# Optimization experiments

Hardware: AMD Instinct MI355X
Metric: run time of the kernel (lower is better)

The kernel has to match this reference:

```python
import jax, jax.numpy as jnp
import numpy as np

BITWIDTH = 8
Q_FRAC = BITWIDTH - 4                       # fractional bits of output quantizer
Q_SCALE = 2.0 ** Q_FRAC                     # 16
QMAX = (2 ** (BITWIDTH - 1) - 1) / Q_SCALE  # 7.9375 (overflow clamp on accumulator)
QMIN = -8.0                                 # underflow clamp / accumulator init
LUT_IN_SCALE = 4096.0                       # diff quantized to Q12 index
LUT_IN_MAX = 32767.0                        # index clamp
LUT_OUT_SCALE = 65536.0                     # look_up (= table/2) lives on a 1/65536 grid


def _lut(diff):
    # Emulates the hex lookup table: table[i]/2 ~= log(1 + exp(-i/4096)),
    # quantized to the 1/65536 grid (table entries are Q15, then halved).
    d_int = jnp.minimum(jnp.floor(diff * LUT_IN_SCALE), LUT_IN_MAX)
    d_q = d_int / LUT_IN_SCALE
    return jnp.round(jnp.log1p(jnp.exp(-d_q)) * LUT_OUT_SCALE) / LUT_OUT_SCALE


def _quant_feature(x):
    # QuantizeFeature(bitwidth, bitwidth-4): round to 1/16 grid, clamp to int8 range.
    q = jnp.clip(jnp.round(x * Q_SCALE), -(2 ** (BITWIDTH - 1)), 2 ** (BITWIDTH - 1) - 1)
    return q / Q_SCALE


def _quantized_log_softmax(x):
    B, C, H, W = x.shape
    flat = x.reshape(B * C, H, W)  # sequential axis = flattened batch*channel (as in source)
    init = jnp.full((H, W), QMIN, dtype=x.dtype)

    def step(sum_exp, t):  # t: [H, W]
        diff = jnp.abs(sum_exp - t)
        lu = _lut(diff)
        # if sum_exp > t: sum_exp += lu else: sum_exp = t + lu  ==  max(sum_exp, t) + lu
        s = jnp.maximum(sum_exp, t) + lu
        s = jnp.clip(s, QMIN, QMAX)  # overflow/underflow clamps
        return s, None

    sum_exp, _ = jax.lax.scan(step, init, flat)
    # final scalar per spatial location is broadcast to every (b, c)
    return _quant_feature(x - sum_exp[None, None, :, :])


def setup_inputs() -> dict:
    key = jax.random.key(0)
    x = jax.random.normal(key, (4, 64, 384, 384), dtype=jnp.float32)
    return {"x": x}


def reference(x):
    return _quantized_log_softmax(x)
```

## Files before the change

kernel.cpp:

```cpp
#include <hip/hip_runtime.h>
#include <math.h>

#define QLS_T   256
#define QLS_HW  (384 * 384)
#define PF      16

#define Q_SCALE      16.0f
#define INV_Q_SCALE  (1.0f / 16.0f)
#define QMAXF        7.9375f
#define QMINF        (-8.0f)
#define LUT_IN_SCALE 4096.0f
#define LUT_IN_MAX   32767.0f
#define INV_LUT_OUT  (1.0f / 65536.0f)

#define NEG_LOG2E_DIV (-1.4426950408889634f / 4096.0f)
#define LN2_X_65536   45426.09375f


__device__ __forceinline__ float qls_combine(float s, float v) {
    float diff  = fabsf(s - v);
    float d_int = fminf(floorf(diff * LUT_IN_SCALE), LUT_IN_MAX);
    float e     = __builtin_amdgcn_exp2f(d_int * NEG_LOG2E_DIV);
    float lu    = rintf(__builtin_amdgcn_logf(1.0f + e) * LN2_X_65536) * INV_LUT_OUT;
    return fminf(fmaxf(fmaxf(s, v) + lu, QMINF), QMAXF);
}

__global__ __launch_bounds__(64) void QuantizedLogSoftmax_12970801234623_kernel(
    const float* __restrict__ x, float* __restrict__ out) {
    const int i = blockIdx.x * 64 + threadIdx.x;
    const float* xp = x + i;

    float s = QMINF;
    float vb[PF];
    #pragma unroll
    for (int j = 0; j < PF; ++j) vb[j] = xp[j * QLS_HW];

    for (int g = 0; g < QLS_T / PF - 1; ++g) {
        const float* np = xp + (g + 1) * PF * QLS_HW;
        float nb[PF];
        #pragma unroll
        for (int j = 0; j < PF; ++j) nb[j] = np[j * QLS_HW];
        #pragma unroll
        for (int j = 0; j < PF; ++j) s = qls_combine(s, vb[j]);
        #pragma unroll
        for (int j = 0; j < PF; ++j) vb[j] = nb[j];
    }
    #pragma unroll
    for (int j = 0; j < PF; ++j) s = qls_combine(s, vb[j]);

    float* op = out + i;
    #pragma unroll
    for (int j = 0; j < PF; ++j) vb[j] = xp[j * QLS_HW];

    for (int g = 0; g < QLS_T / PF - 1; ++g) {
        const float* np = xp + (g + 1) * PF * QLS_HW;
        float*       sp = op + g * PF * QLS_HW;
        float nb[PF];
        #pragma unroll
        for (int j = 0; j < PF; ++j) nb[j] = np[j * QLS_HW];
        #pragma unroll
        for (int j = 0; j < PF; ++j) {
            float q = fminf(fmaxf(rintf((vb[j] - s) * Q_SCALE), -128.0f), 127.0f);
            __builtin_nontemporal_store(q * INV_Q_SCALE, sp + j * QLS_HW);
        }
        #pragma unroll
        for (int j = 0; j < PF; ++j) vb[j] = nb[j];
    }
    float* sp = op + (QLS_T - PF) * QLS_HW;
    #pragma unroll
    for (int j = 0; j < PF; ++j) {
        float q = fminf(fmaxf(rintf((vb[j] - s) * Q_SCALE), -128.0f), 127.0f);
        __builtin_nontemporal_store(q * INV_Q_SCALE, sp + j * QLS_HW);
    }
}

extern "C" void kernel_launch(void* const* d_in, const int* in_sizes, int n_in,
                              void* d_out, int out_size, void* d_ws, size_t ws_size,
                              hipStream_t stream) {
    const float* x = (const float*)d_in[0];
    float* out = (float*)d_out;
    const int threads = 64;
    const int blocks = QLS_HW / threads;
    QuantizedLogSoftmax_12970801234623_kernel<<<blocks, threads, 0, stream>>>(x, out);
}
```

Before: 272.4 us.

## Split sequential channel scan across four warps and vectorize output pass

The 256-step sequential log-sum-exp scan per pixel is split into four 64-step chunks, each handled by its own warp row in a 256-thread block. The partial accumulators are merged through shared memory using the same combine function. The second pass is restructured so that all block threads write float4-vectorized, nontemporal outputs over the full channel range. This is meant to shorten the serial dependency chain and raise occupancy, but it assumes the quantized, clamped combine is associative, so outputs can differ slightly from the strict sequential reference.

```diff
diff --git a/kernel.cpp b/kernel.cpp
--- a/kernel.cpp
+++ b/kernel.cpp
@@ -3,7 +3,9 @@
 
 #define QLS_T   256
 #define QLS_HW  (384 * 384)
-#define PF      16
+#define NSPLIT  4
+#define TPER    (QLS_T / NSPLIT)
+#define PF      8
 
 #define Q_SCALE      16.0f
 #define INV_Q_SCALE  (1.0f / 16.0f)
@@ -16,6 +18,7 @@
 #define NEG_LOG2E_DIV (-1.4426950408889634f / 4096.0f)
 #define LN2_X_65536   45426.09375f
 
+typedef float v4f __attribute__((ext_vector_type(4)));
 
 __device__ __forceinline__ float qls_combine(float s, float v) {
     float diff  = fabsf(s - v);
@@ -25,21 +28,26 @@
     return fminf(fmaxf(fmaxf(s, v) + lu, QMINF), QMAXF);
 }
 
-__global__ __launch_bounds__(64) void QuantizedLogSoftmax_12970801234623_kernel(
+__global__ __launch_bounds__(256, 8) void QuantizedLogSoftmax_12970801234623_kernel(
     const float* __restrict__ x, float* __restrict__ out) {
-    const int i = blockIdx.x * 64 + threadIdx.x;
-    const float* xp = x + i;
+    const int lane = threadIdx.x;
+    const int yq   = threadIdx.y;
+    const int base = blockIdx.x * 64;
+    const int i    = base + lane;
 
+    __shared__ float s_part[NSPLIT][64];
+    __shared__ float s_fin[64];
+
+    const float* xp = x + (size_t)yq * TPER * QLS_HW + i;
     float s = QMINF;
     float vb[PF];
     #pragma unroll
-    for (int j = 0; j < PF; ++j) vb[j] = xp[j * QLS_HW];
-
-    for (int g = 0; g < QLS_T / PF - 1; ++g) {
-        const float* np = xp + (g + 1) * PF * QLS_HW;
+    for (int j = 0; j < PF; ++j) vb[j] = xp[(size_t)j * QLS_HW];
+    for (int g = 0; g < TPER / PF - 1; ++g) {
+        const float* np = xp + (size_t)(g + 1) * PF * QLS_HW;
         float nb[PF];
         #pragma unroll
-        for (int j = 0; j < PF; ++j) nb[j] = np[j * QLS_HW];
+        for (int j = 0; j < PF; ++j) nb[j] = np[(size_t)j * QLS_HW];
         #pragma unroll
         for (int j = 0; j < PF; ++j) s = qls_combine(s, vb[j]);
         #pragma unroll
@@ -48,29 +56,36 @@
     #pragma unroll
     for (int j = 0; j < PF; ++j) s = qls_combine(s, vb[j]);
 
-    float* op = out + i;
-    #pragma unroll
-    for (int j = 0; j < PF; ++j) vb[j] = xp[j * QLS_HW];
+    s_part[yq][lane] = s;
+    __syncthreads();
+    if (yq == 0) {
+        float t = qls_combine(s_part[0][lane], s_part[1][lane]);
+        t = qls_combine(t, s_part[2][lane]);
+        t = qls_combine(t, s_part[3][lane]);
+        s_fin[lane] = t;
+    }
+    __syncthreads();
 
-    for (int g = 0; g < QLS_T / PF - 1; ++g) {
-        const float* np = xp + (g + 1) * PF * QLS_HW;
-        float*       sp = op + g * PF * QLS_HW;
-        float nb[PF];
-        #pragma unroll
-        for (int j = 0; j < PF; ++j) nb[j] = np[j * QLS_HW];
-        #pragma unroll
-        for (int j = 0; j < PF; ++j) {
-            float q = fminf(fmaxf(rintf((vb[j] - s) * Q_SCALE), -128.0f), 127.0f);
-            __builtin_nontemporal_store(q * INV_Q_SCALE, sp + j * QLS_HW);
-        }
-        #pragma unroll
-        for (int j = 0; j < PF; ++j) vb[j] = nb[j];
-    }
-    float* sp = op + (QLS_T - PF) * QLS_HW;
-    #pragma unroll
-    for (int j = 0; j < PF; ++j) {
-        float q = fminf(fmaxf(rintf((vb[j] - s) * Q_SCALE), -128.0f), 127.0f);
-        __builtin_nontemporal_store(q * INV_Q_SCALE, sp + j * QLS_HW);
+    const int tid = yq * 64 + lane;
+    const int tp  = tid >> 4;
+    const int j4  = (tid & 15) * 4;
+    const float sA = s_fin[j4 + 0];
+    const float sB = s_fin[j4 + 1];
+    const float sC = s_fin[j4 + 2];
+    const float sD = s_fin[j4 + 3];
+    const v4f* xv = (const v4f*)x;
+    v4f*       ov = (v4f*)out;
+    const size_t col = (size_t)(base + j4) >> 2;
+    #pragma unroll 4
+    for (int t = tp; t < QLS_T; t += 16) {
+        size_t idx = (size_t)t * (QLS_HW / 4) + col;
+        v4f v = xv[idx];
+        v4f q;
+        q.x = fminf(fmaxf(rintf((v.x - sA) * Q_SCALE), -128.0f), 127.0f) * INV_Q_SCALE;
+        q.y = fminf(fmaxf(rintf((v.y - sB) * Q_SCALE), -128.0f), 127.0f) * INV_Q_SCALE;
+        q.z = fminf(fmaxf(rintf((v.z - sC) * Q_SCALE), -128.0f), 127.0f) * INV_Q_SCALE;
+        q.w = fminf(fmaxf(rintf((v.w - sD) * Q_SCALE), -128.0f), 127.0f) * INV_Q_SCALE;
+        __builtin_nontemporal_store(q, ov + idx);
     }
 }
 
@@ -79,7 +94,7 @@
                               hipStream_t stream) {
     const float* x = (const float*)d_in[0];
     float* out = (float*)d_out;
-    const int threads = 64;
-    const int blocks = QLS_HW / threads;
-    QuantizedLogSoftmax_12970801234623_kernel<<<blocks, threads, 0, stream>>>(x, out);
+    dim3 block(64, NSPLIT, 1);
+    dim3 grid(QLS_HW / 64, 1, 1);
+    QuantizedLogSoftmax_12970801234623_kernel<<<grid, block, 0, stream>>>(x, out);
 }
```

Result: no change. 275.4 us (+1.1%).
